# Performance work log

Hardware: AMD Instinct MI355X
Metric: run time of the kernel (lower is better)

## Reference

```python
import jax, jax.numpy as jnp
import numpy as np

B, T, D_IN, H, D_OUT = 4096, 512, 10, 20, 2


def setup_inputs() -> dict:
    key = jax.random.key(0)
    ks = jax.random.split(key, 12)
    s = 1.0 / np.sqrt(H)  # PyTorch-style uniform bound scale (use normal*s)
    return {
        "x": jax.random.normal(ks[0], (B, T, D_IN), jnp.float32),
        "w_ih0": jax.random.normal(ks[1], (H, D_IN), jnp.float32) * s,
        "w_hh0": jax.random.normal(ks[2], (H, H), jnp.float32) * s,
        "b_ih0": jax.random.normal(ks[3], (H,), jnp.float32) * s,
        "b_hh0": jax.random.normal(ks[4], (H,), jnp.float32) * s,
        "w_ih1": jax.random.normal(ks[5], (H, H), jnp.float32) * s,
        "w_hh1": jax.random.normal(ks[6], (H, H), jnp.float32) * s,
        "b_ih1": jax.random.normal(ks[7], (H,), jnp.float32) * s,
        "b_hh1": jax.random.normal(ks[8], (H,), jnp.float32) * s,
        "fc_w": jax.random.normal(ks[9], (D_OUT, H), jnp.float32) * s,
        "fc_b": jax.random.normal(ks[10], (D_OUT,), jnp.float32) * s,
    }


def _rnn_layer(inp, w_ih, w_hh, b_ih, b_hh):
    # inp: [B, T, Din]. Precompute input projection once (batched GEMM),
    # then scan the sequential recurrence: h_t = tanh(x_t W_ih^T + b_ih + h_{t-1} W_hh^T + b_hh)
    xp = jnp.einsum('btd,hd->bth', inp, w_ih) + (b_ih + b_hh)  # [B, T, H]

    def step(h, xt):
        h = jnp.tanh(xt + h @ w_hh.T)
        return h, h

    h0 = jnp.zeros((inp.shape[0], w_hh.shape[0]), inp.dtype)
    _, hs = jax.lax.scan(step, h0, jnp.swapaxes(xp, 0, 1))  # hs: [T, B, H]
    return jnp.swapaxes(hs, 0, 1)  # [B, T, H]


def reference(x, w_ih0, w_hh0, b_ih0, b_hh0, w_ih1, w_hh1, b_ih1, b_hh1, fc_w, fc_b):
    h1 = _rnn_layer(x, w_ih0, w_hh0, b_ih0, b_hh0)
    h2 = _rnn_layer(h1, w_ih1, w_hh1, b_ih1, b_hh1)
    last = h2[:, -1, :]  # [B, H]
    return last @ fc_w.T + fc_b  # [B, D_OUT]
```

## Files before the change

kernel.cpp:

```cpp
#include <hip/hip_runtime.h>
#include <cstdint>

constexpr int B_   = 4096;
constexpr int T_   = 512;
constexpr int DIN  = 10;
constexpr int H_   = 20;
constexpr int DOUT = 2;

constexpr int SPW = 3;
constexpr int CH  = 2;
constexpr int XV  = CH * DIN / 4;

#define CFENCE() asm volatile("" ::: "memory")
#define PIN(v)   asm volatile("" : "+v"(v))

__device__ __forceinline__ float fast_tanh(float v) {
    float e = __builtin_amdgcn_exp2f(v * 2.885390082f);
    float r = __builtin_amdgcn_rcpf(e + 1.0f);
    return fmaf(-2.0f, r, 1.0f);
}

extern "C" __global__ void __launch_bounds__(64, 1)
rnn_fused(const float* __restrict__ x,
          const float* __restrict__ w_ih0, const float* __restrict__ w_hh0,
          const float* __restrict__ b_ih0, const float* __restrict__ b_hh0,
          const float* __restrict__ w_ih1, const float* __restrict__ w_hh1,
          const float* __restrict__ b_ih1, const float* __restrict__ b_hh1,
          const float* __restrict__ fc_w, const float* __restrict__ fc_b,
          float* __restrict__ out)
{
    const int lane = threadIdx.x;
    const int sl   = lane / H_;
    const int i    = lane - sl * H_;
    const int samp = blockIdx.x * SPW + sl;
    const int sc   = (samp < B_) ? samp : (B_ - 1);
    const int slc  = (sl < SPW) ? sl : SPW;

    __shared__ __align__(16) float h1s[SPW + 1][H_];
    __shared__ __align__(16) float h2s[SPW + 1][H_];

    float wi0[DIN];
    {
        const float2* p = reinterpret_cast<const float2*>(w_ih0 + i * DIN);
        #pragma unroll
        for (int k = 0; k < DIN / 2; ++k) {
            float2 v = p[k];
            wi0[2 * k] = v.x; wi0[2 * k + 1] = v.y;
        }
    }
    float wh0[H_], wi1[H_], wh1[H_];
    {
        const float4* p0 = reinterpret_cast<const float4*>(w_hh0 + i * H_);
        const float4* p1 = reinterpret_cast<const float4*>(w_ih1 + i * H_);
        const float4* p2 = reinterpret_cast<const float4*>(w_hh1 + i * H_);
        #pragma unroll
        for (int k = 0; k < H_ / 4; ++k) {
            float4 a = p0[k]; wh0[4*k]=a.x; wh0[4*k+1]=a.y; wh0[4*k+2]=a.z; wh0[4*k+3]=a.w;
            float4 b = p1[k]; wi1[4*k]=b.x; wi1[4*k+1]=b.y; wi1[4*k+2]=b.z; wi1[4*k+3]=b.w;
            float4 c = p2[k]; wh1[4*k]=c.x; wh1[4*k+1]=c.y; wh1[4*k+2]=c.z; wh1[4*k+3]=c.w;
        }
    }
    float bias0 = b_ih0[i] + b_hh0[i];
    float bias1 = b_ih1[i] + b_hh1[i];

    #pragma unroll
    for (int k = 0; k < DIN; ++k) PIN(wi0[k]);
    #pragma unroll
    for (int k = 0; k < H_; ++k)  PIN(wh0[k]);
    #pragma unroll
    for (int k = 0; k < H_; ++k)  PIN(wi1[k]);
    #pragma unroll
    for (int k = 0; k < H_; ++k)  PIN(wh1[k]);
    PIN(bias0); PIN(bias1);

    float4 h1q[H_ / 4], h2q[H_ / 4];
    #pragma unroll
    for (int k = 0; k < H_ / 4; ++k) {
        h1q[k] = make_float4(0.f, 0.f, 0.f, 0.f);
        h2q[k] = make_float4(0.f, 0.f, 0.f, 0.f);
    }

    const float4* xb = reinterpret_cast<const float4*>(x + (size_t)sc * (T_ * DIN));

    float4 xv[XV];
    #pragma unroll
    for (int k = 0; k < XV; ++k) xv[k] = xb[k];

    for (int t0 = 0; t0 < T_; t0 += CH) {
        float xp[CH];
        #pragma unroll
        for (int m = 0; m < CH; ++m) xp[m] = bias0;
        #pragma unroll
        for (int k = 0; k < XV; ++k) {
            int idx = 4 * k;
            xp[(idx+0)/DIN] = fmaf(xv[k].x, wi0[(idx+0)%DIN], xp[(idx+0)/DIN]);
            xp[(idx+1)/DIN] = fmaf(xv[k].y, wi0[(idx+1)%DIN], xp[(idx+1)/DIN]);
            xp[(idx+2)/DIN] = fmaf(xv[k].z, wi0[(idx+2)%DIN], xp[(idx+2)/DIN]);
            xp[(idx+3)/DIN] = fmaf(xv[k].w, wi0[(idx+3)%DIN], xp[(idx+3)/DIN]);
        }

        {
            const int t0n = (t0 + CH < T_) ? (t0 + CH) : 0;
            #pragma unroll
            for (int k = 0; k < XV; ++k) xv[k] = xb[(t0n * DIN) / 4 + k];
        }

        #pragma unroll
        for (int m = 0; m < CH; ++m) {
            float a0 = xp[m], a1 = 0.f, a2 = 0.f, a3 = 0.f;
            #pragma unroll
            for (int k = 0; k < H_ / 4; ++k) {
                a0 = fmaf(h1q[k].x, wh0[4*k+0], a0);
                a1 = fmaf(h1q[k].y, wh0[4*k+1], a1);
                a2 = fmaf(h1q[k].z, wh0[4*k+2], a2);
                a3 = fmaf(h1q[k].w, wh0[4*k+3], a3);
            }
            float h1n = fast_tanh((a0 + a1) + (a2 + a3));

            CFENCE();
            h1s[slc][i] = h1n;
            CFENCE();

            float b0 = bias1, b1 = 0.f, b2 = 0.f, b3 = 0.f;
            #pragma unroll
            for (int k = 0; k < H_ / 4; ++k) {
                b0 = fmaf(h2q[k].x, wh1[4*k+0], b0);
                b1 = fmaf(h2q[k].y, wh1[4*k+1], b1);
                b2 = fmaf(h2q[k].z, wh1[4*k+2], b2);
                b3 = fmaf(h2q[k].w, wh1[4*k+3], b3);
            }

            #pragma unroll
            for (int k = 0; k < H_ / 4; ++k)
                h1q[k] = reinterpret_cast<const float4*>(&h1s[slc][0])[k];
            CFENCE();

            #pragma unroll
            for (int k = 0; k < H_ / 4; ++k) {
                b0 = fmaf(h1q[k].x, wi1[4*k+0], b0);
                b1 = fmaf(h1q[k].y, wi1[4*k+1], b1);
                b2 = fmaf(h1q[k].z, wi1[4*k+2], b2);
                b3 = fmaf(h1q[k].w, wi1[4*k+3], b3);
            }
            float h2n = fast_tanh((b0 + b1) + (b2 + b3));

            CFENCE();
            h2s[slc][i] = h2n;
            CFENCE();
            #pragma unroll
            for (int k = 0; k < H_ / 4; ++k)
                h2q[k] = reinterpret_cast<const float4*>(&h2s[slc][0])[k];
            CFENCE();
        }
    }

    if (sl < SPW && samp < B_ && i < DOUT) {
        float hf[H_];
        #pragma unroll
        for (int k = 0; k < H_ / 4; ++k) {
            hf[4*k+0] = h2q[k].x; hf[4*k+1] = h2q[k].y;
            hf[4*k+2] = h2q[k].z; hf[4*k+3] = h2q[k].w;
        }
        float acc = fc_b[i];
        #pragma unroll
        for (int j = 0; j < H_; ++j) acc = fmaf(hf[j], fc_w[i * H_ + j], acc);
        out[samp * DOUT + i] = acc;
    }
}

extern "C" void kernel_launch(void* const* d_in, const int* in_sizes, int n_in,
                              void* d_out, int out_size, void* d_ws, size_t ws_size,
                              hipStream_t stream) {
    (void)in_sizes; (void)n_in; (void)d_ws; (void)ws_size; (void)out_size;
    const float* x     = (const float*)d_in[0];
    const float* w_ih0 = (const float*)d_in[1];
    const float* w_hh0 = (const float*)d_in[2];
    const float* b_ih0 = (const float*)d_in[3];
    const float* b_hh0 = (const float*)d_in[4];
    const float* w_ih1 = (const float*)d_in[5];
    const float* w_hh1 = (const float*)d_in[6];
    const float* b_ih1 = (const float*)d_in[7];
    const float* b_hh1 = (const float*)d_in[8];
    const float* fc_w  = (const float*)d_in[9];
    const float* fc_b  = (const float*)d_in[10];
    float* out = (float*)d_out;

    const int grid = (B_ + SPW - 1) / SPW;
    hipLaunchKernelGGL(rnn_fused, dim3(grid), dim3(64), 0, stream,
                       x, w_ih0, w_hh0, b_ih0, b_hh0,
                       w_ih1, w_hh1, b_ih1, b_hh1, fc_w, fc_b, out);
}
```

Baseline: 165.6 us.

## Skew layer-1 and layer-2 recurrences by one timestep to shorten dependency chain

```diff
diff --git a/kernel.cpp b/kernel.cpp
--- a/kernel.cpp
+++ b/kernel.cpp
@@ -8,11 +8,10 @@
 constexpr int DOUT = 2;
 
 constexpr int SPW = 3;
-constexpr int CH  = 2;
+constexpr int CH  = 4;
 constexpr int XV  = CH * DIN / 4;
 
 #define CFENCE() asm volatile("" ::: "memory")
-#define PIN(v)   asm volatile("" : "+v"(v))
 
 __device__ __forceinline__ float fast_tanh(float v) {
     float e = __builtin_amdgcn_exp2f(v * 2.885390082f);
@@ -21,13 +20,13 @@
 }
 
 extern "C" __global__ void __launch_bounds__(64, 1)
-rnn_fused(const float* __restrict__ x,
-          const float* __restrict__ w_ih0, const float* __restrict__ w_hh0,
-          const float* __restrict__ b_ih0, const float* __restrict__ b_hh0,
-          const float* __restrict__ w_ih1, const float* __restrict__ w_hh1,
-          const float* __restrict__ b_ih1, const float* __restrict__ b_hh1,
-          const float* __restrict__ fc_w, const float* __restrict__ fc_b,
-          float* __restrict__ out)
+rnn_skew(const float* __restrict__ x,
+         const float* __restrict__ w_ih0, const float* __restrict__ w_hh0,
+         const float* __restrict__ b_ih0, const float* __restrict__ b_hh0,
+         const float* __restrict__ w_ih1, const float* __restrict__ w_hh1,
+         const float* __restrict__ b_ih1, const float* __restrict__ b_hh1,
+         const float* __restrict__ fc_w, const float* __restrict__ fc_b,
+         float* __restrict__ out)
 {
     const int lane = threadIdx.x;
     const int sl   = lane / H_;
@@ -60,18 +59,8 @@
             float4 c = p2[k]; wh1[4*k]=c.x; wh1[4*k+1]=c.y; wh1[4*k+2]=c.z; wh1[4*k+3]=c.w;
         }
     }
-    float bias0 = b_ih0[i] + b_hh0[i];
-    float bias1 = b_ih1[i] + b_hh1[i];
-
-    #pragma unroll
-    for (int k = 0; k < DIN; ++k) PIN(wi0[k]);
-    #pragma unroll
-    for (int k = 0; k < H_; ++k)  PIN(wh0[k]);
-    #pragma unroll
-    for (int k = 0; k < H_; ++k)  PIN(wi1[k]);
-    #pragma unroll
-    for (int k = 0; k < H_; ++k)  PIN(wh1[k]);
-    PIN(bias0); PIN(bias1);
+    const float bias0 = b_ih0[i] + b_hh0[i];
+    const float bias1 = b_ih1[i] + b_hh1[i];
 
     float4 h1q[H_ / 4], h2q[H_ / 4];
     #pragma unroll
@@ -86,8 +75,43 @@
     #pragma unroll
     for (int k = 0; k < XV; ++k) xv[k] = xb[k];
 
-    for (int t0 = 0; t0 < T_; t0 += CH) {
-        float xp[CH];
+    auto full_step = [&](float xpm) {
+        float a0 = xpm, a1 = 0.f, a2 = 0.f, a3 = 0.f;
+        float b0 = bias1, b1 = 0.f, b2 = 0.f, b3 = 0.f;
+        #pragma unroll
+        for (int k = 0; k < H_ / 4; ++k) {
+            a0 = fmaf(h1q[k].x, wh0[4*k+0], a0);
+            a1 = fmaf(h1q[k].y, wh0[4*k+1], a1);
+            a2 = fmaf(h1q[k].z, wh0[4*k+2], a2);
+            a3 = fmaf(h1q[k].w, wh0[4*k+3], a3);
+            b0 = fmaf(h1q[k].x, wi1[4*k+0], b0);
+            b1 = fmaf(h1q[k].y, wi1[4*k+1], b1);
+            b2 = fmaf(h1q[k].z, wi1[4*k+2], b2);
+            b3 = fmaf(h1q[k].w, wi1[4*k+3], b3);
+        }
+        #pragma unroll
+        for (int k = 0; k < H_ / 4; ++k) {
+            b0 = fmaf(h2q[k].x, wh1[4*k+0], b0);
+            b1 = fmaf(h2q[k].y, wh1[4*k+1], b1);
+            b2 = fmaf(h2q[k].z, wh1[4*k+2], b2);
+            b3 = fmaf(h2q[k].w, wh1[4*k+3], b3);
+        }
+        float h1n = fast_tanh((a0 + a1) + (a2 + a3));
+        float h2n = fast_tanh((b0 + b1) + (b2 + b3));
+        CFENCE();
+        h1s[slc][i] = h1n;
+        h2s[slc][i] = h2n;
+        CFENCE();
+        #pragma unroll
+        for (int k = 0; k < H_ / 4; ++k)
+            h1q[k] = reinterpret_cast<const float4*>(&h1s[slc][0])[k];
+        #pragma unroll
+        for (int k = 0; k < H_ / 4; ++k)
+            h2q[k] = reinterpret_cast<const float4*>(&h2s[slc][0])[k];
+        CFENCE();
+    };
+
+    auto consume_xp = [&](float* xp) {
         #pragma unroll
         for (int m = 0; m < CH; ++m) xp[m] = bias0;
         #pragma unroll
@@ -98,60 +122,63 @@
             xp[(idx+2)/DIN] = fmaf(xv[k].z, wi0[(idx+2)%DIN], xp[(idx+2)/DIN]);
             xp[(idx+3)/DIN] = fmaf(xv[k].w, wi0[(idx+3)%DIN], xp[(idx+3)/DIN]);
         }
-
+    };
+
+    {
+        float xp[CH];
+        consume_xp(xp);
+        #pragma unroll
+        for (int k = 0; k < XV; ++k) xv[k] = xb[(CH * DIN) / 4 + k];
+
+        float h1n = fast_tanh(xp[0]);
+        CFENCE();
+        h1s[slc][i] = h1n;
+        CFENCE();
+        #pragma unroll
+        for (int k = 0; k < H_ / 4; ++k)
+            h1q[k] = reinterpret_cast<const float4*>(&h1s[slc][0])[k];
+        CFENCE();
+
+        #pragma unroll
+        for (int m = 1; m < CH; ++m) full_step(xp[m]);
+    }
+
+    for (int t0 = CH; t0 < T_; t0 += CH) {
+        float xp[CH];
+        consume_xp(xp);
         {
             const int t0n = (t0 + CH < T_) ? (t0 + CH) : 0;
             #pragma unroll
             for (int k = 0; k < XV; ++k) xv[k] = xb[(t0n * DIN) / 4 + k];
         }
-
-        #pragma unroll
-        for (int m = 0; m < CH; ++m) {
-            float a0 = xp[m], a1 = 0.f, a2 = 0.f, a3 = 0.f;
-            #pragma unroll
-            for (int k = 0; k < H_ / 4; ++k) {
-                a0 = fmaf(h1q[k].x, wh0[4*k+0], a0);
-                a1 = fmaf(h1q[k].y, wh0[4*k+1], a1);
-                a2 = fmaf(h1q[k].z, wh0[4*k+2], a2);
-                a3 = fmaf(h1q[k].w, wh0[4*k+3], a3);
-            }
-            float h1n = fast_tanh((a0 + a1) + (a2 + a3));
-
-            CFENCE();
-            h1s[slc][i] = h1n;
-            CFENCE();
-
-            float b0 = bias1, b1 = 0.f, b2 = 0.f, b3 = 0.f;
-            #pragma unroll
-            for (int k = 0; k < H_ / 4; ++k) {
-                b0 = fmaf(h2q[k].x, wh1[4*k+0], b0);
-                b1 = fmaf(h2q[k].y, wh1[4*k+1], b1);
-                b2 = fmaf(h2q[k].z, wh1[4*k+2], b2);
-                b3 = fmaf(h2q[k].w, wh1[4*k+3], b3);
-            }
-
-            #pragma unroll
-            for (int k = 0; k < H_ / 4; ++k)
-                h1q[k] = reinterpret_cast<const float4*>(&h1s[slc][0])[k];
-            CFENCE();
-
-            #pragma unroll
-            for (int k = 0; k < H_ / 4; ++k) {
-                b0 = fmaf(h1q[k].x, wi1[4*k+0], b0);
-                b1 = fmaf(h1q[k].y, wi1[4*k+1], b1);
-                b2 = fmaf(h1q[k].z, wi1[4*k+2], b2);
-                b3 = fmaf(h1q[k].w, wi1[4*k+3], b3);
-            }
-            float h2n = fast_tanh((b0 + b1) + (b2 + b3));
-
-            CFENCE();
-            h2s[slc][i] = h2n;
-            CFENCE();
-            #pragma unroll
-            for (int k = 0; k < H_ / 4; ++k)
-                h2q[k] = reinterpret_cast<const float4*>(&h2s[slc][0])[k];
-            CFENCE();
-        }
+        #pragma unroll
+        for (int m = 0; m < CH; ++m) full_step(xp[m]);
+    }
+
+    {
+        float b0 = bias1, b1 = 0.f, b2 = 0.f, b3 = 0.f;
+        #pragma unroll
+        for (int k = 0; k < H_ / 4; ++k) {
+            b0 = fmaf(h1q[k].x, wi1[4*k+0], b0);
+            b1 = fmaf(h1q[k].y, wi1[4*k+1], b1);
+            b2 = fmaf(h1q[k].z, wi1[4*k+2], b2);
+            b3 = fmaf(h1q[k].w, wi1[4*k+3], b3);
+        }
+        #pragma unroll
+        for (int k = 0; k < H_ / 4; ++k) {
+            b0 = fmaf(h2q[k].x, wh1[4*k+0], b0);
+            b1 = fmaf(h2q[k].y, wh1[4*k+1], b1);
+            b2 = fmaf(h2q[k].z, wh1[4*k+2], b2);
+            b3 = fmaf(h2q[k].w, wh1[4*k+3], b3);
+        }
+        float h2n = fast_tanh((b0 + b1) + (b2 + b3));
+        CFENCE();
+        h2s[slc][i] = h2n;
+        CFENCE();
+        #pragma unroll
+        for (int k = 0; k < H_ / 4; ++k)
+            h2q[k] = reinterpret_cast<const float4*>(&h2s[slc][0])[k];
+        CFENCE();
     }
 
     if (sl < SPW && samp < B_ && i < DOUT) {
@@ -186,7 +213,7 @@
     float* out = (float*)d_out;
 
     const int grid = (B_ + SPW - 1) / SPW;
-    hipLaunchKernelGGL(rnn_fused, dim3(grid), dim3(64), 0, stream,
+    hipLaunchKernelGGL(rnn_skew, dim3(grid), dim3(64), 0, stream,
                        x, w_ih0, w_hh0, b_ih0, b_hh0,
                        w_ih1, w_hh1, b_ih1, b_hh1, fc_w, fc_b, out);
 }
```

After: 154.3 us. 6.8% less time.
